# Kernel tuning notes

Measured on AMD Instinct MI355X. Metric: run time of the kernel, lower is better.

Reference implementation:

```python
import jax, jax.numpy as jnp
import numpy as np

N = 50000      # nodes
E = 800000     # edges (avg degree 16)
IN = 128       # in_feats
HID = 32       # hidden_feats per head
H = 4          # num_heads
NEG_SLOPE = 0.2


def setup_inputs() -> dict:
    key = jax.random.key(0)
    ks = jax.random.split(key, 13)
    x = jax.random.normal(ks[0], (N, IN), jnp.float32)
    src = jax.random.randint(ks[1], (E,), 0, N, jnp.int32)
    dst = jax.random.randint(ks[2], (E,), 0, N, jnp.int32)

    def lin(k, fi, fo):
        return jax.random.normal(k, (fi, fo), jnp.float32) * (1.0 / np.sqrt(fi))

    # conv1: IN -> H*HID
    W1 = lin(ks[3], IN, H * HID)
    al1 = jax.random.normal(ks[4], (H, HID), jnp.float32) * 0.1
    ar1 = jax.random.normal(ks[5], (H, HID), jnp.float32) * 0.1
    b1 = jnp.zeros((H, HID), jnp.float32)
    # conv2: H*HID -> H*HID
    W2 = lin(ks[6], H * HID, H * HID)
    al2 = jax.random.normal(ks[7], (H, HID), jnp.float32) * 0.1
    ar2 = jax.random.normal(ks[8], (H, HID), jnp.float32) * 0.1
    b2 = jnp.zeros((H, HID), jnp.float32)
    # fc: HID -> 1
    fcW = lin(ks[9], HID, 1)
    fcb = jnp.zeros((1,), jnp.float32)
    return {"x": x, "src": src, "dst": dst,
            "W1": W1, "al1": al1, "ar1": ar1, "b1": b1,
            "W2": W2, "al2": al2, "ar2": ar2, "b2": b2,
            "fcW": fcW, "fcb": fcb}


def gat_conv(x, src, dst, W, al, ar, b):
    # x: [N, F_in] -> feat: [N, H, HID]
    feat = (x @ W).reshape(N, H, HID)
    el = jnp.sum(feat * al, axis=-1)            # [N, H]
    er = jnp.sum(feat * ar, axis=-1)            # [N, H]
    e = jax.nn.leaky_relu(el[src] + er[dst], NEG_SLOPE)  # [E, H]
    # segment softmax over incoming edges of each dst node
    m = jax.ops.segment_max(e, dst, num_segments=N)      # [N, H]
    ex = jnp.exp(e - m[dst])                              # [E, H]
    denom = jax.ops.segment_sum(ex, dst, num_segments=N)  # [N, H]
    alpha = ex / denom[dst]                                # [E, H]
    msg = feat[src] * alpha[:, :, None]                    # [E, H, HID]
    out = jax.ops.segment_sum(msg, dst, num_segments=N)   # [N, H, HID]
    return out + b[None, :, :]


def reference(x, src, dst, W1, al1, ar1, b1, W2, al2, ar2, b2, fcW, fcb):
    h = gat_conv(x, src, dst, W1, al1, ar1, b1).reshape(N, H * HID)
    h = jax.nn.relu(h)
    # dropout(0.5) is identity in eval mode
    h = gat_conv(h, src, dst, W2, al2, ar2, b2).mean(axis=1)  # [N, HID]
    return h @ fcW + fcb                                       # [N, 1]
```

## Files before the change

### kernel.cpp

```cpp
#include <hip/hip_runtime.h>
#include <hip/hip_fp16.h>

#define LEAK 0.2f
#define CAP 64
#define CS 16

static __device__ inline int swz(int c, int j) {
    int qb = j >> 3, r = j & 7;
    return c * 144 + qb * 8 + (qb >> 2) * 4 + r;
}
static __device__ inline unsigned q4(float4 v, float is) {
    int x0 = __float2int_rn(v.x * is) + 128; x0 = min(max(x0, 0), 255);
    int x1 = __float2int_rn(v.y * is) + 128; x1 = min(max(x1, 0), 255);
    int x2 = __float2int_rn(v.z * is) + 128; x2 = min(max(x2, 0), 255);
    int x3 = __float2int_rn(v.w * is) + 128; x3 = min(max(x3, 0), 255);
    return (unsigned)x0 | ((unsigned)x1 << 8) | ((unsigned)x2 << 16) | ((unsigned)x3 << 24);
}

__global__ __launch_bounds__(256) void k0(
    int* __restrict__ cnt,
    const float* __restrict__ W2, const float* __restrict__ al2,
    const float* __restrict__ ar2, const float* __restrict__ fcW,
    const float* __restrict__ b2, float* __restrict__ WfT,
    float* __restrict__ bc, int N, int zb) {
    const int b = blockIdx.x;
    const int t = threadIdx.x;
    if (b < zb) {
        int i = b * 256 + t;
        if (i < N * (CS / 4)) ((int4*)cnt)[i] = make_int4(0, 0, 0, 0);
        return;
    }
    int idx = (b - zb) * 256 + t;
    if (idx < 1536) {
        int c = idx >> 7, k = idx & 127;
        int h = c & 3, sel = c >> 2;
        const float* vec = (sel == 0) ? (al2 + 32 * h)
                         : (sel == 1) ? (ar2 + 32 * h) : fcW;
        float s = 0.f;
#pragma unroll 8
        for (int m = 0; m < 32; m++) s += W2[k * 128 + 32 * h + m] * vec[m];
        WfT[c * 128 + k] = s;
    } else if (idx < 1540) {
        int h = idx - 1536;
        float s = 0.f;
        for (int m = 0; m < 32; m++) s += b2[h * 32 + m] * fcW[m];
        bc[h] = s;
    }
}

__global__ __launch_bounds__(256, 4) void k_eg(
    const float* __restrict__ X, const float* __restrict__ W,
    const float* __restrict__ al, const float* __restrict__ ar,
    float2* __restrict__ elsc2, float* __restrict__ er_nh,
    unsigned* __restrict__ fq8,
    const int* __restrict__ src, const int* __restrict__ dst,
    int* __restrict__ cnt, unsigned short* __restrict__ ell,
    int N, int E, int R, int GO, int T) {
    __shared__ float sW[32 * 128];
    __shared__ float sXT[32 * 64];
    const int b = blockIdx.x;
    const int t = threadIdx.x;
    const int o = b >> 3;
    const int g0 = (o * GO) / T;
    const bool isGemm = ((o + 1) * GO) / T > g0;

    if (!isGemm) {
        const int part = b & 7;
        const int rank = o - g0;
        const int S = (N + 7) >> 3;
        const int lo = part * S;
        const int hi = (lo + S < N) ? (lo + S) : N;
        const int per = (E + R - 1) / R;
        const int e0 = rank * per;
        const int e1 = (e0 + per < E) ? (e0 + per) : E;
        int e = e0 + t;
        for (; e + 768 < e1; e += 1024) {
            int d0 = dst[e];       int d1 = dst[e + 256];
            int d2 = dst[e + 512]; int d3 = dst[e + 768];
            if (d0 >= lo && d0 < hi) {
                int pos = atomicAdd(&cnt[d0 * CS], 1);
                if (pos < CAP) ell[(size_t)d0 * CAP + pos] = (unsigned short)src[e];
            }
            if (d1 >= lo && d1 < hi) {
                int pos = atomicAdd(&cnt[d1 * CS], 1);
                if (pos < CAP) ell[(size_t)d1 * CAP + pos] = (unsigned short)src[e + 256];
            }
            if (d2 >= lo && d2 < hi) {
                int pos = atomicAdd(&cnt[d2 * CS], 1);
                if (pos < CAP) ell[(size_t)d2 * CAP + pos] = (unsigned short)src[e + 512];
            }
            if (d3 >= lo && d3 < hi) {
                int pos = atomicAdd(&cnt[d3 * CS], 1);
                if (pos < CAP) ell[(size_t)d3 * CAP + pos] = (unsigned short)src[e + 768];
            }
        }
        for (; e < e1; e += 256) {
            int d = dst[e];
            if (d >= lo && d < hi) {
                int pos = atomicAdd(&cnt[d * CS], 1);
                if (pos < CAP) ell[(size_t)d * CAP + pos] = (unsigned short)src[e];
            }
        }
        return;
    }

    const int tile = g0 * 8 + (b & 7);
    const int r0 = tile * 64;
    if (r0 >= N) return;
    const int tx = t & 15;
    const int ty = t >> 4;
    const float4* X4 = (const float4*)X;
    const float4* W4 = (const float4*)W;
    float4* sW4 = (float4*)sW;
    const float4* sXT4 = (const float4*)sXT;

    float4 acc[4][2];
#pragma unroll
    for (int r = 0; r < 4; r++) {
        acc[r][0] = make_float4(0.f, 0.f, 0.f, 0.f);
        acc[r][1] = make_float4(0.f, 0.f, 0.f, 0.f);
    }
    for (int ks = 0; ks < 4; ++ks) {
        if (ks) __syncthreads();
#pragma unroll
        for (int i = 0; i < 4; i++) {
            int idx = i * 256 + t;
            sW4[idx] = W4[1024 * ks + idx];
        }
#pragma unroll
        for (int i = 0; i < 2; i++) {
            int idx = i * 256 + t;
            int row = idx >> 3;
            int kq = idx & 7;
            float4 v = make_float4(0.f, 0.f, 0.f, 0.f);
            if (r0 + row < N) v = X4[(size_t)(r0 + row) * 32 + ks * 8 + kq];
            int sc = ((row >> 2) ^ kq) * 4 + (row & 3);
            sXT[(4 * kq + 0) * 64 + sc] = v.x;
            sXT[(4 * kq + 1) * 64 + sc] = v.y;
            sXT[(4 * kq + 2) * 64 + sc] = v.z;
            sXT[(4 * kq + 3) * 64 + sc] = v.w;
        }
        __syncthreads();
#pragma unroll 4
        for (int k = 0; k < 32; k++) {
            float4 w0 = sW4[k * 32 + tx];
            float4 w1 = sW4[k * 32 + 16 + tx];
            float4 x0 = sXT4[k * 16 + (ty ^ (k >> 2))];
            float xs[4] = {x0.x, x0.y, x0.z, x0.w};
#pragma unroll
            for (int r = 0; r < 4; r++) {
                acc[r][0].x += xs[r] * w0.x; acc[r][0].y += xs[r] * w0.y;
                acc[r][0].z += xs[r] * w0.z; acc[r][0].w += xs[r] * w0.w;
                acc[r][1].x += xs[r] * w1.x; acc[r][1].y += xs[r] * w1.y;
                acc[r][1].z += xs[r] * w1.z; acc[r][1].w += xs[r] * w1.w;
            }
        }
    }
    const float4* al4p = (const float4*)al;
    const float4* ar4p = (const float4*)ar;
    float4 alA = al4p[tx], alB = al4p[16 + tx];
    float4 arA = ar4p[tx], arB = ar4p[16 + tx];
#pragma unroll
    for (int r = 0; r < 4; r++) {
        int row = r0 + ty * 4 + r;
        bool ok = row < N;
        float4 a0 = acc[r][0], a1 = acc[r][1];
        float m = fmaxf(fmaxf(fmaxf(fabsf(a0.x), fabsf(a0.y)),
                              fmaxf(fabsf(a0.z), fabsf(a0.w))),
                        fmaxf(fmaxf(fabsf(a1.x), fabsf(a1.y)),
                              fmaxf(fabsf(a1.z), fabsf(a1.w))));
#pragma unroll
        for (int off = 1; off < 16; off <<= 1) m = fmaxf(m, __shfl_xor(m, off));
        float scale = m * (1.f / 127.f);
        float is = (m > 0.f) ? (127.f / m) : 0.f;
        if (ok) {
            fq8[(size_t)row * 32 + tx] = q4(a0, is);
            fq8[(size_t)row * 32 + 16 + tx] = q4(a1, is);
        }
        float elA = a0.x * alA.x + a0.y * alA.y + a0.z * alA.z + a0.w * alA.w;
        float erA = a0.x * arA.x + a0.y * arA.y + a0.z * arA.z + a0.w * arA.w;
        float elB = a1.x * alB.x + a1.y * alB.y + a1.z * alB.z + a1.w * alB.w;
        float erB = a1.x * arB.x + a1.y * arB.y + a1.z * arB.z + a1.w * arB.w;
#pragma unroll
        for (int off = 1; off < 8; off <<= 1) {
            elA += __shfl_xor(elA, off); erA += __shfl_xor(erA, off);
            elB += __shfl_xor(elB, off); erB += __shfl_xor(erB, off);
        }
        if (ok && tx == 0) {
            elsc2[row * 4 + 0] = make_float2(elA, scale);
            elsc2[row * 4 + 2] = make_float2(elB, scale);
            er_nh[row * 4 + 0] = erA;
            er_nh[row * 4 + 2] = erB;
        }
        if (ok && tx == 8) {
            elsc2[row * 4 + 1] = make_float2(elA, scale);
            elsc2[row * 4 + 3] = make_float2(elB, scale);
            er_nh[row * 4 + 1] = erA;
            er_nh[row * 4 + 3] = erB;
        }
    }
}

__global__ __launch_bounds__(256) void k_agg1P(
    const unsigned* __restrict__ fq8, const float2* __restrict__ elsc2,
    const float* __restrict__ er_nh, const unsigned short* __restrict__ ell,
    const int* __restrict__ cnt, const float* __restrict__ b1,
    const float* __restrict__ WfT, float2* __restrict__ Pag,
    float* __restrict__ er2, int N) {
    __shared__ float sWf[12 * 144];
    for (int i = threadIdx.x; i < 1536; i += 256)
        sWf[swz(i >> 7, i & 127)] = WfT[i];
    __syncthreads();
    const int wave = threadIdx.x >> 6, lane = threadIdx.x & 63;
    const int nsub = lane >> 4, q = lane & 15, h = q >> 2;
    const int wbase = q * 8 + (q >> 2) * 4;
    const uint2* fq2 = (const uint2*)fq8;

    const int n = blockIdx.x * 16 + wave * 4 + nsub;
    const bool nok = n < N;
    const int nc = nok ? n : (N - 1);
    int deg = nok ? cnt[n * CS] : 0; if (deg > CAP) deg = CAP;
    float er = nok ? er_nh[n * 4 + h] : 0.f;
    const unsigned short* row = ell + (size_t)nc * CAP;

    int dm = deg;
    dm = max(dm, __shfl_xor(dm, 16));
    dm = max(dm, __shfl_xor(dm, 32));

    float acc[8] = {0.f, 0.f, 0.f, 0.f, 0.f, 0.f, 0.f, 0.f};
    float den = 0.f, wss = 0.f;
    for (int jt = 0; jt < dm; jt += 16) {
        int s_all = (jt + q < CAP) ? (int)row[jt + q] : 0;
        int lim = dm - jt; if (lim > 16) lim = 16;
        for (int u = 0; u < lim; u += 8) {
            int sv[8]; float2 esv[8]; uint2 fv[8];
#pragma unroll
            for (int v = 0; v < 8; v++) {
                int jj = jt + u + v;
                int s = __shfl(s_all, (lane & 48) | ((u + v) & 15));
                sv[v] = (jj < deg) ? s : 0;
            }
#pragma unroll
            for (int v = 0; v < 8; v++) esv[v] = elsc2[sv[v] * 4 + h];
#pragma unroll
            for (int v = 0; v < 8; v++) fv[v] = fq2[(size_t)sv[v] * 16 + q];
#pragma unroll
            for (int v = 0; v < 8; v++) {
                int jj = jt + u + v;
                bool valid = jj < deg;
                float e = esv[v].x + er;
                e = fmaxf(e, LEAK * e);
                float w = valid ? __expf(e) : 0.f;
                float ws = w * esv[v].y;
                unsigned ua = fv[v].x, ub = fv[v].y;
                acc[0] += ws * (float)(ua & 0xff);
                acc[1] += ws * (float)((ua >> 8) & 0xff);
                acc[2] += ws * (float)((ua >> 16) & 0xff);
                acc[3] += ws * (float)(ua >> 24);
                acc[4] += ws * (float)(ub & 0xff);
                acc[5] += ws * (float)((ub >> 8) & 0xff);
                acc[6] += ws * (float)((ub >> 16) & 0xff);
                acc[7] += ws * (float)(ub >> 24);
                den += w; wss += ws;
            }
        }
    }
    float inv = (den > 0.f) ? (1.f / den) : 0.f;
    float off128 = 128.f * wss;
    float4 b1a = ((const float4*)b1)[q * 2];
    float4 b1b = ((const float4*)b1)[q * 2 + 1];
    float hv[8];
    hv[0] = fmaxf((acc[0] - off128) * inv + b1a.x, 0.f);
    hv[1] = fmaxf((acc[1] - off128) * inv + b1a.y, 0.f);
    hv[2] = fmaxf((acc[2] - off128) * inv + b1a.z, 0.f);
    hv[3] = fmaxf((acc[3] - off128) * inv + b1a.w, 0.f);
    hv[4] = fmaxf((acc[4] - off128) * inv + b1b.x, 0.f);
    hv[5] = fmaxf((acc[5] - off128) * inv + b1b.y, 0.f);
    hv[6] = fmaxf((acc[6] - off128) * inv + b1b.z, 0.f);
    hv[7] = fmaxf((acc[7] - off128) * inv + b1b.w, 0.f);
    float p[12];
#pragma unroll
    for (int c = 0; c < 12; c++) {
        const float* wr = sWf + c * 144 + wbase;
        float4 wa = *(const float4*)wr;
        float4 wb = *(const float4*)(wr + 4);
        p[c] = hv[0] * wa.x + hv[1] * wa.y + hv[2] * wa.z + hv[3] * wa.w
             + hv[4] * wb.x + hv[5] * wb.y + hv[6] * wb.z + hv[7] * wb.w;
    }
#pragma unroll
    for (int off = 1; off < 16; off <<= 1) {
#pragma unroll
        for (int c = 0; c < 12; c++) p[c] += __shfl_xor(p[c], off);
    }
    if (nok) {
        if (q < 4) Pag[(size_t)n * 4 + q] = make_float2(p[q], p[8 + q]);
        else if (q < 8) er2[(size_t)n * 4 + (q - 4)] = p[q];
    }
}

__global__ __launch_bounds__(256) void k_agg2(
    const float2* __restrict__ Pag, const float* __restrict__ er2,
    const unsigned short* __restrict__ ell, const int* __restrict__ cnt,
    const float* __restrict__ bc, const float* __restrict__ fcb,
    float* __restrict__ out, int N) {
    int idx = blockIdx.x * 256 + threadIdx.x;
    int n = idx >> 2, h = idx & 3;
    if (n >= N) return;
    int deg = cnt[n * CS]; if (deg > CAP) deg = CAP;
    float er = er2[(size_t)n * 4 + h];
    const unsigned short* row = ell + (size_t)n * CAP;
    float num = 0.f, den = 0.f;
    int j = 0, d8 = deg & ~7;
    for (; j < d8; j += 8) {
        ushort4 sa = *(const ushort4*)(row + j);
        ushort4 sb = *(const ushort4*)(row + j + 4);
        int sv[8] = {sa.x, sa.y, sa.z, sa.w, sb.x, sb.y, sb.z, sb.w};
        float2 g[8];
#pragma unroll
        for (int v = 0; v < 8; v++) g[v] = Pag[(size_t)sv[v] * 4 + h];
#pragma unroll
        for (int v = 0; v < 8; v++) {
            float e = g[v].x + er; e = fmaxf(e, LEAK * e);
            float w = __expf(e);
            num += w * g[v].y; den += w;
        }
    }
    for (; j < deg; ++j) {
        int s = row[j];
        float2 gg = Pag[(size_t)s * 4 + h];
        float e = gg.x + er; e = fmaxf(e, LEAK * e);
        float w = __expf(e);
        num += w * gg.y; den += w;
    }
    float r = (den > 0.f) ? (num / den) : 0.f;
    r += bc[h];
    r += __shfl_xor(r, 1);
    r += __shfl_xor(r, 2);
    if (h == 0) out[n] = 0.25f * r + fcb[0];
}

extern "C" void kernel_launch(void* const* d_in, const int* in_sizes, int n_in,
                              void* d_out, int out_size, void* d_ws, size_t ws_size,
                              hipStream_t stream) {
    const float* x   = (const float*)d_in[0];
    const int* src   = (const int*)d_in[1];
    const int* dst   = (const int*)d_in[2];
    const float* W1  = (const float*)d_in[3];
    const float* al1 = (const float*)d_in[4];
    const float* ar1 = (const float*)d_in[5];
    const float* b1  = (const float*)d_in[6];
    const float* W2  = (const float*)d_in[7];
    const float* al2 = (const float*)d_in[8];
    const float* ar2 = (const float*)d_in[9];
    const float* b2  = (const float*)d_in[10];
    const float* fcW = (const float*)d_in[11];
    const float* fcb = (const float*)d_in[12];
    float* out = (float*)d_out;

    const int N = in_sizes[0] / 128;
    const int E = in_sizes[1];

    char* w = (char*)d_ws;
    size_t off = 0;
    auto alloc = [&](size_t bytes) {
        void* p = w + off;
        off = (off + bytes + 255) & ~(size_t)255;
        return p;
    };
    unsigned* fq8  = (unsigned*)alloc((size_t)N * 32 * 4);
    float2* elsc2  = (float2*)alloc((size_t)N * 4 * 8);
    float* er_nh   = (float*)alloc((size_t)N * 4 * 4);
    float2* Pag    = (float2*)alloc((size_t)N * 4 * 8);
    float* er2     = (float*)alloc((size_t)N * 4 * 4);
    float* WfT     = (float*)alloc((size_t)(12 * 128 + 4) * 4);
    float* bc      = WfT + 12 * 128;
    int* cnt       = (int*)alloc((size_t)N * CS * 4);
    unsigned short* ell = (unsigned short*)alloc((size_t)N * CAP * 2);

    const int zb = (N * (CS / 4) + 255) / 256;
    const int gtiles = (N + 63) / 64;
    const int R = 256;
    const int GO = (gtiles + 7) / 8;
    const int T = R + GO;

    k0<<<zb + 7, 256, 0, stream>>>(
        cnt, W2, al2, ar2, fcW, b2, WfT, bc, N, zb);
    k_eg<<<8 * T, 256, 0, stream>>>(
        x, W1, al1, ar1, elsc2, er_nh, fq8,
        src, dst, cnt, ell, N, E, R, GO, T);
    k_agg1P<<<(N + 15) / 16, 256, 0, stream>>>(
        fq8, elsc2, er_nh, ell, cnt, b1, WfT, Pag, er2, N);
    k_agg2<<<(N * 4 + 255) / 256, 256, 0, stream>>>(
        Pag, er2, ell, cnt, bc, fcb, out, N);
}
```

Baseline: 188.6 us.

## Pack src/dst into 32-bit edge words and vectorize ELL row loads in aggregation

A pre-pass in k0 packs each edge's dst and src into one 32-bit word, so the eight-way partitioned ELL build reads 4 bytes per edge per pass instead of reading dst and then src separately. k_agg1P now loads each node's whole 64-entry ELL row once as uint2 per lane and extracts neighbour indices with shuffles, replacing the per-tile row loads and the max-degree reduction. k_agg2 loads the full 128-byte row as eight uint4 and loops with per-lane early exit. The trade-offs are an extra E*4-byte buffer and an extra pass over the edge lists, and the packing assumes node ids fit in 16 bits.

```diff
diff --git a/kernel.cpp b/kernel.cpp
--- a/kernel.cpp
+++ b/kernel.cpp
@@ -19,10 +19,12 @@
 
 __global__ __launch_bounds__(256) void k0(
     int* __restrict__ cnt,
+    const int* __restrict__ src, const int* __restrict__ dst,
+    unsigned* __restrict__ pk,
     const float* __restrict__ W2, const float* __restrict__ al2,
     const float* __restrict__ ar2, const float* __restrict__ fcW,
     const float* __restrict__ b2, float* __restrict__ WfT,
-    float* __restrict__ bc, int N, int zb) {
+    float* __restrict__ bc, int N, int E, int zb, int pkb) {
     const int b = blockIdx.x;
     const int t = threadIdx.x;
     if (b < zb) {
@@ -30,7 +32,20 @@
         if (i < N * (CS / 4)) ((int4*)cnt)[i] = make_int4(0, 0, 0, 0);
         return;
     }
-    int idx = (b - zb) * 256 + t;
+    if (b < zb + pkb) {
+        int i = (b - zb) * 256 + t;
+        int e0 = i * 4;
+        if (e0 + 3 < E) {
+            int4 d = ((const int4*)dst)[i];
+            int4 s = ((const int4*)src)[i];
+            ((int4*)pk)[i] = make_int4((d.x << 16) | s.x, (d.y << 16) | s.y,
+                                       (d.z << 16) | s.z, (d.w << 16) | s.w);
+        } else if (e0 < E) {
+            for (int e = e0; e < E; e++) pk[e] = ((unsigned)dst[e] << 16) | (unsigned)src[e];
+        }
+        return;
+    }
+    int idx = (b - zb - pkb) * 256 + t;
     if (idx < 1536) {
         int c = idx >> 7, k = idx & 127;
         int h = c & 3, sel = c >> 2;
@@ -53,7 +68,7 @@
     const float* __restrict__ al, const float* __restrict__ ar,
     float2* __restrict__ elsc2, float* __restrict__ er_nh,
     unsigned* __restrict__ fq8,
-    const int* __restrict__ src, const int* __restrict__ dst,
+    const unsigned* __restrict__ pk,
     int* __restrict__ cnt, unsigned short* __restrict__ ell,
     int N, int E, int R, int GO, int T) {
     __shared__ float sW[32 * 128];
@@ -75,30 +90,33 @@
         const int e1 = (e0 + per < E) ? (e0 + per) : E;
         int e = e0 + t;
         for (; e + 768 < e1; e += 1024) {
-            int d0 = dst[e];       int d1 = dst[e + 256];
-            int d2 = dst[e + 512]; int d3 = dst[e + 768];
+            unsigned p0 = pk[e];       unsigned p1 = pk[e + 256];
+            unsigned p2 = pk[e + 512]; unsigned p3 = pk[e + 768];
+            int d0 = (int)(p0 >> 16), d1 = (int)(p1 >> 16);
+            int d2 = (int)(p2 >> 16), d3 = (int)(p3 >> 16);
             if (d0 >= lo && d0 < hi) {
                 int pos = atomicAdd(&cnt[d0 * CS], 1);
-                if (pos < CAP) ell[(size_t)d0 * CAP + pos] = (unsigned short)src[e];
+                if (pos < CAP) ell[(size_t)d0 * CAP + pos] = (unsigned short)(p0 & 0xffffu);
             }
             if (d1 >= lo && d1 < hi) {
                 int pos = atomicAdd(&cnt[d1 * CS], 1);
-                if (pos < CAP) ell[(size_t)d1 * CAP + pos] = (unsigned short)src[e + 256];
+                if (pos < CAP) ell[(size_t)d1 * CAP + pos] = (unsigned short)(p1 & 0xffffu);
             }
             if (d2 >= lo && d2 < hi) {
                 int pos = atomicAdd(&cnt[d2 * CS], 1);
-                if (pos < CAP) ell[(size_t)d2 * CAP + pos] = (unsigned short)src[e + 512];
+                if (pos < CAP) ell[(size_t)d2 * CAP + pos] = (unsigned short)(p2 & 0xffffu);
             }
             if (d3 >= lo && d3 < hi) {
                 int pos = atomicAdd(&cnt[d3 * CS], 1);
-                if (pos < CAP) ell[(size_t)d3 * CAP + pos] = (unsigned short)src[e + 768];
+                if (pos < CAP) ell[(size_t)d3 * CAP + pos] = (unsigned short)(p3 & 0xffffu);
             }
         }
         for (; e < e1; e += 256) {
-            int d = dst[e];
+            unsigned p = pk[e];
+            int d = (int)(p >> 16);
             if (d >= lo && d < hi) {
                 int pos = atomicAdd(&cnt[d * CS], 1);
-                if (pos < CAP) ell[(size_t)d * CAP + pos] = (unsigned short)src[e];
+                if (pos < CAP) ell[(size_t)d * CAP + pos] = (unsigned short)(p & 0xffffu);
             }
         }
         return;
@@ -219,50 +237,43 @@
     const int n = blockIdx.x * 16 + wave * 4 + nsub;
     const bool nok = n < N;
     const int nc = nok ? n : (N - 1);
-    int deg = nok ? cnt[n * CS] : 0; if (deg > CAP) deg = CAP;
-    float er = nok ? er_nh[n * 4 + h] : 0.f;
+    int deg = nok ? cnt[nc * CS] : 0; if (deg > CAP) deg = CAP;
+    float er = nok ? er_nh[nc * 4 + h] : 0.f;
     const unsigned short* row = ell + (size_t)nc * CAP;
-
-    int dm = deg;
-    dm = max(dm, __shfl_xor(dm, 16));
-    dm = max(dm, __shfl_xor(dm, 32));
+    uint2 rv = ((const uint2*)row)[q];
 
     float acc[8] = {0.f, 0.f, 0.f, 0.f, 0.f, 0.f, 0.f, 0.f};
     float den = 0.f, wss = 0.f;
-    for (int jt = 0; jt < dm; jt += 16) {
-        int s_all = (jt + q < CAP) ? (int)row[jt + q] : 0;
-        int lim = dm - jt; if (lim > 16) lim = 16;
-        for (int u = 0; u < lim; u += 8) {
-            int sv[8]; float2 esv[8]; uint2 fv[8];
-#pragma unroll
-            for (int v = 0; v < 8; v++) {
-                int jj = jt + u + v;
-                int s = __shfl(s_all, (lane & 48) | ((u + v) & 15));
-                sv[v] = (jj < deg) ? s : 0;
-            }
-#pragma unroll
-            for (int v = 0; v < 8; v++) esv[v] = elsc2[sv[v] * 4 + h];
-#pragma unroll
-            for (int v = 0; v < 8; v++) fv[v] = fq2[(size_t)sv[v] * 16 + q];
-#pragma unroll
-            for (int v = 0; v < 8; v++) {
-                int jj = jt + u + v;
-                bool valid = jj < deg;
-                float e = esv[v].x + er;
-                e = fmaxf(e, LEAK * e);
-                float w = valid ? __expf(e) : 0.f;
-                float ws = w * esv[v].y;
-                unsigned ua = fv[v].x, ub = fv[v].y;
-                acc[0] += ws * (float)(ua & 0xff);
-                acc[1] += ws * (float)((ua >> 8) & 0xff);
-                acc[2] += ws * (float)((ua >> 16) & 0xff);
-                acc[3] += ws * (float)(ua >> 24);
-                acc[4] += ws * (float)(ub & 0xff);
-                acc[5] += ws * (float)((ub >> 8) & 0xff);
-                acc[6] += ws * (float)((ub >> 16) & 0xff);
-                acc[7] += ws * (float)(ub >> 24);
-                den += w; wss += ws;
-            }
+    for (int j0 = 0; j0 < deg; j0 += 8) {
+        int sv[8]; float2 esv[8]; uint2 fv[8];
+#pragma unroll
+        for (int v = 0; v < 8; v++) {
+            int wrd = __shfl((int)((v & 2) ? rv.y : rv.x),
+                             (lane & 48) | ((j0 >> 2) + (v >> 2)));
+            int s = (v & 1) ? ((wrd >> 16) & 0xffff) : (wrd & 0xffff);
+            sv[v] = (j0 + v < deg) ? s : 0;
+        }
+#pragma unroll
+        for (int v = 0; v < 8; v++) esv[v] = elsc2[sv[v] * 4 + h];
+#pragma unroll
+        for (int v = 0; v < 8; v++) fv[v] = fq2[(size_t)sv[v] * 16 + q];
+#pragma unroll
+        for (int v = 0; v < 8; v++) {
+            bool valid = (j0 + v) < deg;
+            float e = esv[v].x + er;
+            e = fmaxf(e, LEAK * e);
+            float w = valid ? __expf(e) : 0.f;
+            float ws = w * esv[v].y;
+            unsigned ua = fv[v].x, ub = fv[v].y;
+            acc[0] += ws * (float)(ua & 0xff);
+            acc[1] += ws * (float)((ua >> 8) & 0xff);
+            acc[2] += ws * (float)((ua >> 16) & 0xff);
+            acc[3] += ws * (float)(ua >> 24);
+            acc[4] += ws * (float)(ub & 0xff);
+            acc[5] += ws * (float)((ub >> 8) & 0xff);
+            acc[6] += ws * (float)((ub >> 16) & 0xff);
+            acc[7] += ws * (float)(ub >> 24);
+            den += w; wss += ws;
         }
     }
     float inv = (den > 0.f) ? (1.f / den) : 0.f;
@@ -308,29 +319,36 @@
     if (n >= N) return;
     int deg = cnt[n * CS]; if (deg > CAP) deg = CAP;
     float er = er2[(size_t)n * 4 + h];
-    const unsigned short* row = ell + (size_t)n * CAP;
+    const uint4* row4 = (const uint4*)(ell + (size_t)n * CAP);
+    uint4 rv[8];
+#pragma unroll
+    for (int i = 0; i < 8; i++) rv[i] = row4[i];
+
     float num = 0.f, den = 0.f;
-    int j = 0, d8 = deg & ~7;
-    for (; j < d8; j += 8) {
-        ushort4 sa = *(const ushort4*)(row + j);
-        ushort4 sb = *(const ushort4*)(row + j + 4);
-        int sv[8] = {sa.x, sa.y, sa.z, sa.w, sb.x, sb.y, sb.z, sb.w};
+#pragma unroll
+    for (int b8 = 0; b8 < 8; ++b8) {
+        int j0 = b8 * 8;
+        if (j0 >= deg) break;
+        int sv[8];
+#pragma unroll
+        for (int v = 0; v < 8; v++) {
+            unsigned wrd = ((v >> 1) == 0) ? rv[b8].x
+                         : ((v >> 1) == 1) ? rv[b8].y
+                         : ((v >> 1) == 2) ? rv[b8].z : rv[b8].w;
+            int s = (v & 1) ? (int)(wrd >> 16) : (int)(wrd & 0xffffu);
+            sv[v] = (j0 + v < deg) ? s : 0;
+        }
         float2 g[8];
 #pragma unroll
         for (int v = 0; v < 8; v++) g[v] = Pag[(size_t)sv[v] * 4 + h];
 #pragma unroll
         for (int v = 0; v < 8; v++) {
-            float e = g[v].x + er; e = fmaxf(e, LEAK * e);
-            float w = __expf(e);
-            num += w * g[v].y; den += w;
-        }
-    }
-    for (; j < deg; ++j) {
-        int s = row[j];
-        float2 gg = Pag[(size_t)s * 4 + h];
-        float e = gg.x + er; e = fmaxf(e, LEAK * e);
-        float w = __expf(e);
-        num += w * gg.y; den += w;
+            if (j0 + v < deg) {
+                float e = g[v].x + er; e = fmaxf(e, LEAK * e);
+                float w = __expf(e);
+                num += w * g[v].y; den += w;
+            }
+        }
     }
     float r = (den > 0.f) ? (num / den) : 0.f;
     r += bc[h];
@@ -376,18 +394,20 @@
     float* bc      = WfT + 12 * 128;
     int* cnt       = (int*)alloc((size_t)N * CS * 4);
     unsigned short* ell = (unsigned short*)alloc((size_t)N * CAP * 2);
+    unsigned* pk   = (unsigned*)alloc((size_t)E * 4);
 
     const int zb = (N * (CS / 4) + 255) / 256;
+    const int pkb = (E / 4 + 255) / 256;
     const int gtiles = (N + 63) / 64;
     const int R = 256;
     const int GO = (gtiles + 7) / 8;
     const int T = R + GO;
 
-    k0<<<zb + 7, 256, 0, stream>>>(
-        cnt, W2, al2, ar2, fcW, b2, WfT, bc, N, zb);
+    k0<<<zb + pkb + 8, 256, 0, stream>>>(
+        cnt, src, dst, pk, W2, al2, ar2, fcW, b2, WfT, bc, N, E, zb, pkb);
     k_eg<<<8 * T, 256, 0, stream>>>(
         x, W1, al1, ar1, elsc2, er_nh, fq8,
-        src, dst, cnt, ell, N, E, R, GO, T);
+        pk, cnt, ell, N, E, R, GO, T);
     k_agg1P<<<(N + 15) / 16, 256, 0, stream>>>(
         fq8, elsc2, er_nh, ell, cnt, b1, WfT, Pag, er2, N);
     k_agg2<<<(N * 4 + 255) / 256, 256, 0, stream>>>(
```

New measurement: 186.5 us (median of 2 runs). Within noise of the previous version (-1.1%).
